# Optimization experiments

Measured on AMD Instinct MI355X. Metric: run time of the kernel, lower is better.

## Reference

```python
import jax, jax.numpy as jnp
import numpy as np

GRID = 64
BIG = 1.0e6  # threshold pushing masked-out pixels to huge distance


def _grid_dist(grid_h, grid_w):
    # pairwise euclidean distance between all grid points, (H, W, H, W)
    xs, ys = jnp.meshgrid(jnp.arange(grid_h), jnp.arange(grid_w), indexing='ij')
    coords = jnp.stack([xs.ravel(), ys.ravel()], axis=-1).astype(jnp.float32)  # (H*W, 2)
    d = jnp.sqrt(jnp.sum((coords[:, None, :] - coords[None, :, :]) ** 2, axis=-1))
    return d.reshape(grid_h, grid_w, grid_h, grid_w)


def setup_inputs() -> dict:
    key = jax.random.key(0)
    k1, k2 = jax.random.split(key)
    gt = jax.random.uniform(k1, (8, 64, 64), dtype=jnp.float32)
    pred = jax.random.uniform(k2, (8, 64, 64), dtype=jnp.float32)
    return {"gt": gt, "pred": pred}


def reference(gt, pred):
    # mode='l2_sq': sum over last axis (W for a (B,H,W) mask), then mean
    loss = jnp.mean(jnp.sum((gt - pred) ** 2, axis=-1))

    # affinity loss (dist_mat += 1.0 as in the original)
    dist = _grid_dist(GRID, GRID) + 1.0  # (64,64,64,64)

    gt_th = gt + (1.0 - gt) * BIG      # (B,H,W)
    pred_th = pred + (1.0 - pred) * BIG

    # dist_masked[b,h,w,i,j] = gt_th[b,h,w] * dist[h,w,i,j] * pred[b,i,j]
    dist_masked = gt_th[:, :, :, None, None] * dist[None] * pred[:, None, None, :, :]
    min_dist = jnp.mean(jnp.min(dist_masked, axis=(3, 4)))

    dist_masked_inv = pred_th[:, :, :, None, None] * dist[None] * gt[:, None, None, :, :]
    min_dist_inv = jnp.mean(jnp.min(dist_masked_inv, axis=(3, 4)))

    return (loss, min_dist, min_dist_inv)
```

## Files before the change

### kernel.cpp

```cpp
#include <hip/hip_runtime.h>

#define BIGV 1.0e6f

__global__ __launch_bounds__(256) void build_lists(
    const float* __restrict__ gt, const float* __restrict__ pred,
    uint2* __restrict__ lists)
{
    __shared__ int cnt[256];
    __shared__ int off[256];

    const int blk   = blockIdx.x;
    const int b     = blk >> 1;
    const int which = blk & 1;
    const float* __restrict__ src = (which ? gt : pred) + b * 4096;
    uint2* __restrict__ out = lists + blk * 4096;
    const int tid = threadIdx.x;

    cnt[tid] = 0;
    __syncthreads();

    float vals[16];
    int   bkt[16];
    #pragma unroll
    for (int k = 0; k < 16; ++k) {
        const int idx = tid + (k << 8);
        const float v = src[idx];
        vals[k] = v;
        int bb = (int)(v * 256.0f);
        bb = bb > 255 ? 255 : (bb < 0 ? 0 : bb);
        bkt[k] = bb;
        atomicAdd(&cnt[bb], 1);
    }
    __syncthreads();

    if (tid < 64) {
        int carry = 0;
        #pragma unroll
        for (int k = 0; k < 4; ++k) {
            const int x = cnt[k * 64 + tid];
            int incl = x;
            #pragma unroll
            for (int s = 1; s < 64; s <<= 1) {
                int y = __shfl_up(incl, s, 64);
                if (tid >= s) incl += y;
            }
            off[k * 64 + tid] = carry + incl - x;
            carry += __shfl(incl, 63, 64);
        }
    }
    __syncthreads();

    #pragma unroll
    for (int k = 0; k < 16; ++k) {
        const int idx  = tid + (k << 8);
        const int slot = atomicAdd(&off[bkt[k]], 1);
        out[slot] = make_uint2(__float_as_uint(vals[k]), (unsigned)idx);
    }
}

__global__ __launch_bounds__(128) void imageloss_query(
    const float* __restrict__ gt, const float* __restrict__ pred,
    const uint2* __restrict__ lists, float* __restrict__ ws)
{
    const int blk  = blockIdx.x;
    const int b    = blk >> 6;
    const int h    = blk & 63;
    const int tid  = threadIdx.x;
    const int w    = tid & 63;
    const int wave = tid >> 6;

    const uint2* __restrict__ list = lists + (b * 2 + wave) * 4096;
    const float hf = (float)h, wf = (float)w;

    float m = 3.4e38f;
    int e = 0;
    while (true) {
        int e_end = e + 16;
        if (e_end > 4096) e_end = 4096;
        for (; e < e_end; ++e) {
            const uint2 ent = list[e];
            const float v   = __uint_as_float(ent.x);
            const int   idx = (int)ent.y;
            const float dx  = hf - (float)(idx >> 6);
            const float dy  = wf - (float)(idx & 63);
            const float d   = __builtin_amdgcn_sqrtf(fmaf(dy, dy, dx * dx));
            m = fminf(m, fmaf(v, d, v));
        }
        if (e >= 4096) break;
        const float vn = __uint_as_float(list[e].x);
        const float lb = floorf(vn * 256.0f) * (1.0f / 256.0f);
        if (__all(m <= lb)) break;
    }

    const float g = gt[b * 4096 + h * 64 + w];
    const float p = pred[b * 4096 + h * 64 + w];

    if (wave == 0) {
        const float gth = g + (1.0f - g) * BIGV;
        float c1 = gth * m;
        float df = g - p;
        float sq = df * df;
        #pragma unroll
        for (int off = 32; off > 0; off >>= 1) {
            c1 += __shfl_down(c1, off, 64);
            sq += __shfl_down(sq, off, 64);
        }
        if (w == 0) {
            atomicAdd(&ws[0], sq);
            atomicAdd(&ws[1], c1);
        }
    } else {
        const float pth = p + (1.0f - p) * BIGV;
        float c2 = pth * m;
        #pragma unroll
        for (int off = 32; off > 0; off >>= 1)
            c2 += __shfl_down(c2, off, 64);
        if (w == 0) atomicAdd(&ws[2], c2);
    }
}

__global__ void imageloss_final(const float* __restrict__ ws, float* __restrict__ out)
{
    out[0] = ws[0] * (1.0f / 512.0f);
    out[1] = ws[1] * (1.0f / 32768.0f);
    out[2] = ws[2] * (1.0f / 32768.0f);
}

extern "C" void kernel_launch(void* const* d_in, const int* in_sizes, int n_in,
                              void* d_out, int out_size, void* d_ws, size_t ws_size,
                              hipStream_t stream)
{
    const float* gt   = (const float*)d_in[0];
    const float* pred = (const float*)d_in[1];
    float* out = (float*)d_out;
    float* ws  = (float*)d_ws;
    uint2* lists = (uint2*)((char*)d_ws + 1024);

    hipMemsetAsync(ws, 0, 3 * sizeof(float), stream);
    build_lists<<<16, 256, 0, stream>>>(gt, pred, lists);
    imageloss_query<<<512, 128, 0, stream>>>(gt, pred, lists, ws);
    imageloss_final<<<1, 1, 0, stream>>>(ws, out);
}
```

Before: 49.40 us.

## Fuse final reduction into query kernel, use per-wave histograms, dual-accumulator scan

The separate final kernel is removed. The last block to finish, detected with a global atomic counter and a threadfence, now writes the three outputs, which saves one kernel launch. build_lists now keeps per-wave histograms with a block-wide scan, giving a deterministic, wave-ordered scatter and less contention on the LDS atomics. The query loop is unrolled by two with independent min accumulators to add instruction-level parallelism. Risks include the extra atomic counter traffic and a changed element ordering within buckets.

New measurement: 50.69 us. 2.6% more time.

```diff
diff --git a/kernel.cpp b/kernel.cpp
--- a/kernel.cpp
+++ b/kernel.cpp
@@ -6,61 +6,70 @@
     const float* __restrict__ gt, const float* __restrict__ pred,
     uint2* __restrict__ lists)
 {
-    __shared__ int cnt[256];
-    __shared__ int off[256];
+    __shared__ int cnt[4][256];
+    __shared__ int wtot[4];
 
     const int blk   = blockIdx.x;
     const int b     = blk >> 1;
     const int which = blk & 1;
     const float* __restrict__ src = (which ? gt : pred) + b * 4096;
     uint2* __restrict__ out = lists + blk * 4096;
+
     const int tid = threadIdx.x;
+    const int wv  = tid >> 6;
+    const int ln  = tid & 63;
 
-    cnt[tid] = 0;
+    #pragma unroll
+    for (int w = 0; w < 4; ++w) cnt[w][tid] = 0;
     __syncthreads();
 
     float vals[16];
     int   bkt[16];
     #pragma unroll
     for (int k = 0; k < 16; ++k) {
-        const int idx = tid + (k << 8);
+        const int idx = wv * 1024 + k * 64 + ln;
         const float v = src[idx];
         vals[k] = v;
         int bb = (int)(v * 256.0f);
         bb = bb > 255 ? 255 : (bb < 0 ? 0 : bb);
         bkt[k] = bb;
-        atomicAdd(&cnt[bb], 1);
+        atomicAdd(&cnt[wv][bb], 1);
     }
     __syncthreads();
 
-    if (tid < 64) {
-        int carry = 0;
-        #pragma unroll
-        for (int k = 0; k < 4; ++k) {
-            const int x = cnt[k * 64 + tid];
-            int incl = x;
-            #pragma unroll
-            for (int s = 1; s < 64; s <<= 1) {
-                int y = __shfl_up(incl, s, 64);
-                if (tid >= s) incl += y;
-            }
-            off[k * 64 + tid] = carry + incl - x;
-            carry += __shfl(incl, 63, 64);
-        }
+    const int t  = tid;
+    const int c0 = cnt[0][t], c1 = cnt[1][t], c2 = cnt[2][t], c3 = cnt[3][t];
+    const int tot = c0 + c1 + c2 + c3;
+    int incl = tot;
+    #pragma unroll
+    for (int s = 1; s < 64; s <<= 1) {
+        int y = __shfl_up(incl, s, 64);
+        if (ln >= s) incl += y;
     }
+    if (ln == 63) wtot[wv] = incl;
+    __syncthreads();
+    int carry = 0;
+    #pragma unroll
+    for (int w = 0; w < 4; ++w) carry += (w < wv) ? wtot[w] : 0;
+    const int P = carry + incl - tot;
+    cnt[0][t] = P;
+    cnt[1][t] = P + c0;
+    cnt[2][t] = P + c0 + c1;
+    cnt[3][t] = P + c0 + c1 + c2;
     __syncthreads();
 
     #pragma unroll
     for (int k = 0; k < 16; ++k) {
-        const int idx  = tid + (k << 8);
-        const int slot = atomicAdd(&off[bkt[k]], 1);
+        const int idx  = wv * 1024 + k * 64 + ln;
+        const int slot = atomicAdd(&cnt[wv][bkt[k]], 1);
         out[slot] = make_uint2(__float_as_uint(vals[k]), (unsigned)idx);
     }
 }
 
 __global__ __launch_bounds__(128) void imageloss_query(
     const float* __restrict__ gt, const float* __restrict__ pred,
-    const uint2* __restrict__ lists, float* __restrict__ ws)
+    const uint2* __restrict__ lists, float* __restrict__ ws,
+    float* __restrict__ out)
 {
     const int blk  = blockIdx.x;
     const int b    = blk >> 6;
@@ -72,28 +81,33 @@
     const uint2* __restrict__ list = lists + (b * 2 + wave) * 4096;
     const float hf = (float)h, wf = (float)w;
 
-    float m = 3.4e38f;
+    float ma = 3.4e38f, mb = 3.4e38f;
     int e = 0;
     while (true) {
-        int e_end = e + 16;
-        if (e_end > 4096) e_end = 4096;
-        for (; e < e_end; ++e) {
-            const uint2 ent = list[e];
-            const float v   = __uint_as_float(ent.x);
-            const int   idx = (int)ent.y;
-            const float dx  = hf - (float)(idx >> 6);
-            const float dy  = wf - (float)(idx & 63);
-            const float d   = __builtin_amdgcn_sqrtf(fmaf(dy, dy, dx * dx));
-            m = fminf(m, fmaf(v, d, v));
+        const int e_end = (e + 16 < 4096) ? e + 16 : 4096;
+        for (; e < e_end; e += 2) {
+            const uint2 ea = list[e];
+            const uint2 eb = list[e + 1];
+            const float va = __uint_as_float(ea.x);
+            const float vb = __uint_as_float(eb.x);
+            const int   ia = (int)ea.y, ib = (int)eb.y;
+            const float dxa = hf - (float)(ia >> 6), dya = wf - (float)(ia & 63);
+            const float dxb = hf - (float)(ib >> 6), dyb = wf - (float)(ib & 63);
+            const float da = __builtin_amdgcn_sqrtf(fmaf(dya, dya, dxa * dxa));
+            const float db = __builtin_amdgcn_sqrtf(fmaf(dyb, dyb, dxb * dxb));
+            ma = fminf(ma, fmaf(va, da, va));
+            mb = fminf(mb, fmaf(vb, db, vb));
         }
         if (e >= 4096) break;
         const float vn = __uint_as_float(list[e].x);
         const float lb = floorf(vn * 256.0f) * (1.0f / 256.0f);
-        if (__all(m <= lb)) break;
+        if (__all(fminf(ma, mb) <= lb)) break;
     }
+    const float m = fminf(ma, mb);
 
-    const float g = gt[b * 4096 + h * 64 + w];
-    const float p = pred[b * 4096 + h * 64 + w];
+    const int cell = b * 4096 + h * 64 + w;
+    const float g = gt[cell];
+    const float p = pred[cell];
 
     if (wave == 0) {
         const float gth = g + (1.0f - g) * BIGV;
@@ -117,13 +131,20 @@
             c2 += __shfl_down(c2, off, 64);
         if (w == 0) atomicAdd(&ws[2], c2);
     }
-}
 
-__global__ void imageloss_final(const float* __restrict__ ws, float* __restrict__ out)
-{
-    out[0] = ws[0] * (1.0f / 512.0f);
-    out[1] = ws[1] * (1.0f / 32768.0f);
-    out[2] = ws[2] * (1.0f / 32768.0f);
+    __syncthreads();
+    if (tid == 0) {
+        __threadfence();
+        const int old = atomicAdd((int*)&ws[3], 1);
+        if (old == 511) {
+            const float s0 = atomicAdd(&ws[0], 0.0f);
+            const float s1 = atomicAdd(&ws[1], 0.0f);
+            const float s2 = atomicAdd(&ws[2], 0.0f);
+            out[0] = s0 * (1.0f / 512.0f);
+            out[1] = s1 * (1.0f / 32768.0f);
+            out[2] = s2 * (1.0f / 32768.0f);
+        }
+    }
 }
 
 extern "C" void kernel_launch(void* const* d_in, const int* in_sizes, int n_in,
@@ -136,8 +157,7 @@
     float* ws  = (float*)d_ws;
     uint2* lists = (uint2*)((char*)d_ws + 1024);
 
-    hipMemsetAsync(ws, 0, 3 * sizeof(float), stream);
+    hipMemsetAsync(ws, 0, 4 * sizeof(float), stream);
     build_lists<<<16, 256, 0, stream>>>(gt, pred, lists);
-    imageloss_query<<<512, 128, 0, stream>>>(gt, pred, lists, ws);
-    imageloss_final<<<1, 1, 0, stream>>>(ws, out);
+    imageloss_query<<<512, 128, 0, stream>>>(gt, pred, lists, ws, out);
 }
```
